# Kernel optimization log

Hardware: AMD Instinct MI355X
Metric: run time of the kernel (lower is better)

Reference implementation:

```python
import jax, jax.numpy as jnp
import numpy as np

L, HS, IN, B, S = 2, 512, 512, 64, 1024

def setup_inputs() -> dict:
    key = jax.random.key(0)
    ks = jax.random.split(key, 11)
    sc = 0.02
    return {
        'x':  jax.random.normal(ks[0], (B, S, IN), jnp.float32),
        'h0': jnp.zeros((L, B, HS), jnp.float32),
        'W1': jax.random.normal(ks[1], (L, 3, 1)) * sc,
        'W2': jax.random.normal(ks[2], (L, HS, IN)) * sc,
        'U1': jax.random.normal(ks[3], (L, 3, 1)) * sc,
        'U2': jax.random.normal(ks[4], (L, HS, HS)) * sc,
        'dW1': jax.random.normal(ks[5], (L, 3, 1)) * sc,
        'dW2': jax.random.normal(ks[6], (L, HS, IN)) * sc,
        'dU1': jax.random.normal(ks[7], (L, 3, 1)) * sc,
        'dU2': jax.random.normal(ks[8], (L, HS, HS)) * sc,
        'b1': jax.random.normal(ks[9], (L, 3 * HS, 1)) * sc,
        'b2': jax.random.normal(ks[10], (L, 3 * HS, 1)) * sc,
    }

def reference(x, h0, W1, W2, U1, U2, dW1, dW2, dU1, dU2, b1, b2):
    # x: (b, s, in); h0: (L, b, HS). All layers read the same x_t (per source).
    b = x.shape[0]
    hs = h0.shape[2]
    bias = b1 + b2                      # (L, 3HS, 1)
    h_init = jnp.transpose(h0, (0, 2, 1))  # (L, HS, b) -- column-major state like gates

    def step(h, x_t):                   # h: (L, HS, b), x_t: (b, in)
        Wx = jnp.einsum('lhi,bi->lhb', W2, x_t)
        dWx = jnp.einsum('lhi,bi->lhb', dW2, x_t)
        Uh = jnp.einsum('lho,lob->lhb', U2, h)
        dUh = jnp.einsum('lho,lob->lhb', dU2, h)
        # kron(A(3,1), M(HS,b)) = stack_g A[g]*M -> (3HS, b)
        gates = (jnp.einsum('lg,lhb->lghb', W1[:, :, 0], Wx)
                 + jnp.einsum('lg,lhb->lghb', U1[:, :, 0], Uh)
                 + jnp.einsum('lg,lhb->lghb', dW1[:, :, 0], dWx)
                 + jnp.einsum('lg,lhb->lghb', dU1[:, :, 0], dUh)
                 ).reshape(h.shape[0], 3 * hs, b) + bias
        r = jax.nn.sigmoid(gates[:, :hs])          # computed but unused, as in source
        z = jax.nn.sigmoid(gates[:, hs:2 * hs])
        n = jnp.tanh(gates[:, 2 * hs:])
        h_new = (1.0 - z) * n + z * h
        return h_new, jnp.transpose(h_new[-1])     # emit last layer, (b, HS)

    h_fin, seq = jax.lax.scan(step, h_init, jnp.transpose(x, (1, 0, 2)))
    hidden_seq = jnp.transpose(seq, (1, 0, 2))     # (b, s, HS)
    state = jnp.transpose(h_fin, (0, 2, 1))        # (L, b, HS)
    return hidden_seq, state
```

## Files before the change

kernel.cpp:

```cpp
#include <hip/hip_runtime.h>


#define HS 512
#define IN_DIM 512
#define BATCH 64
#define SEQ 1024
#define NB 16
#define NDOM 8
#define LDS_ROW 516
#define HROW 520

typedef __attribute__((ext_vector_type(8))) short bf16x8;
typedef __attribute__((ext_vector_type(4))) float f32x4;
typedef unsigned long long u64;
typedef unsigned int u32;
typedef unsigned short ushort_t;

__device__ __forceinline__ ushort_t f2bf(float f) {
  u32 u = __float_as_uint(f);
  u += 0x7FFFu + ((u >> 16) & 1u);
  return (ushort_t)(u >> 16);
}
__device__ __forceinline__ float bf2f(ushort_t s) {
  return __uint_as_float(((u32)s) << 16);
}

__global__ void gru_prep(const float* __restrict__ h0,
                         ushort_t* __restrict__ hbuf,
                         u32* __restrict__ cnt) {
  u32 tid = blockIdx.x * 256u + threadIdx.x;
  if (tid < 2u * BATCH * HS) hbuf[tid] = f2bf(h0[tid]);
  if (tid < NDOM * (SEQ + 1) + 64u) cnt[tid] = 0u;
}

__global__ __launch_bounds__(256, 1) void gru_main(
    const float* __restrict__ x, float* __restrict__ out,
    const float* __restrict__ W1, const float* __restrict__ W2,
    const float* __restrict__ U1, const float* __restrict__ U2,
    const float* __restrict__ dW1, const float* __restrict__ dW2,
    const float* __restrict__ dU1, const float* __restrict__ dU2,
    const float* __restrict__ b1, const float* __restrict__ b2,
    ushort_t* __restrict__ hbuf, u32* __restrict__ cntws) {
  __shared__ __align__(16) float xlds[2][NB * LDS_ROW];
  __shared__ __align__(16) ushort_t hlds[NB * HROW];
  __shared__ u32 mode_sh;

  const int bid    = blockIdx.x;
  const int domain = bid & 7;
  const int slice  = bid >> 3;
  const int layer  = domain & 1;
  const int bg     = domain >> 1;
  const int bo     = bg * NB;
  const int tid    = threadIdx.x;
  const int lane   = tid & 63;
  const int wave   = tid >> 6;
  const int quad   = lane >> 4;
  const int ln     = lane & 15;
  const int hw     = slice * 64 + wave * 16;

  u32* const cnt = cntws + domain * (SEQ + 1);
  u32* const tab = cntws + NDOM * (SEQ + 1);

  if (tid == 0) {
    u32 xcc;
    asm volatile("s_getreg_b32 %0, hwreg(HW_REG_XCC_ID)" : "=s"(xcc));
    __hip_atomic_store(&tab[domain * 8 + slice], 256u + xcc,
                       __ATOMIC_RELAXED, __HIP_MEMORY_SCOPE_AGENT);
    u32 vals[8];
    for (;;) {
      bool ready = true;
#pragma unroll
      for (int i = 0; i < 8; ++i) {
        vals[i] = __hip_atomic_load(&tab[domain * 8 + i],
                                    __ATOMIC_RELAXED, __HIP_MEMORY_SCOPE_AGENT);
        ready = ready && (vals[i] >= 256u);
      }
      if (ready) break;
      __builtin_amdgcn_s_sleep(8);
    }
    u32 m = 1u;
#pragma unroll
    for (int i = 1; i < 8; ++i) m = (vals[i] == vals[0]) ? m : 0u;
    mode_sh = m;
  }
  __syncthreads();
  const bool fast = (mode_sh != 0u);

  const float w1z = W1[layer*3+1], w1n = W1[layer*3+2];
  const float dw1z = dW1[layer*3+1], dw1n = dW1[layer*3+2];
  const float u1z = U1[layer*3+1], u1n = U1[layer*3+2];
  const float du1z = dU1[layer*3+1], du1n = dU1[layer*3+2];
  const int hrow_w = hw + ln;
  const float* W2r  = W2  + ((size_t)layer*HS + hrow_w) * IN_DIM;
  const float* dW2r = dW2 + ((size_t)layer*HS + hrow_w) * IN_DIM;
  const float* U2r  = U2  + ((size_t)layer*HS + hrow_w) * HS;
  const float* dU2r = dU2 + ((size_t)layer*HS + hrow_w) * HS;

  bf16x8 uf[2][16], wf[2][16];
#pragma unroll
  for (int kc = 0; kc < 16; ++kc) {
    const int off = kc*32 + quad*8;
#pragma unroll
    for (int i = 0; i < 8; ++i) {
      float w2 = W2r[off+i], dw2 = dW2r[off+i];
      float u2 = U2r[off+i], du2 = dU2r[off+i];
      wf[0][kc][i] = (short)f2bf(w1z*w2 + dw1z*dw2);
      wf[1][kc][i] = (short)f2bf(w1n*w2 + dw1n*dw2);
      uf[0][kc][i] = (short)f2bf(u1z*u2 + du1z*du2);
      uf[1][kc][i] = (short)f2bf(u1n*u2 + du1n*du2);
    }
  }
  float bz[4], bn[4];
#pragma unroll
  for (int r = 0; r < 4; ++r) {
    const int row = hw + quad*4 + r;
    bz[r] = b1[layer*1536 + 512  + row] + b2[layer*1536 + 512  + row];
    bn[r] = b1[layer*1536 + 1024 + row] + b2[layer*1536 + 1024 + row];
  }

  const int b_lane = bo + ln;
  const size_t slotsz = (size_t)2 * BATCH * HS;
  ushort_t* hl = hbuf + (size_t)layer * BATCH * HS;

#pragma unroll
  for (int i = 0; i < 8; ++i) {
    int bi = wave * 4 + (i >> 1), ch = i & 1;
    const float* g = x + ((size_t)(bo + bi) * SEQ) * IN_DIM + ch * 256 + lane * 4;
    __builtin_amdgcn_global_load_lds(
        (const __attribute__((address_space(1))) void*)g,
        (__attribute__((address_space(3))) void*)&xlds[0][bi * LDS_ROW + ch * 256],
        16, 0, 0);
  }
  asm volatile("s_waitcnt vmcnt(0)" ::: "memory");
  __syncthreads();

  if (fast) {
    for (int t = 0; t < SEQ; ++t) {
      if (t + 1 < SEQ) {
#pragma unroll
        for (int i = 0; i < 8; ++i) {
          int bi = wave * 4 + (i >> 1), ch = i & 1;
          const float* g = x + ((size_t)(bo + bi) * SEQ + (t + 1)) * IN_DIM + ch * 256 + lane * 4;
          __builtin_amdgcn_global_load_lds(
              (const __attribute__((address_space(1))) void*)g,
              (__attribute__((address_space(3))) void*)&xlds[(t + 1) & 1][bi * LDS_ROW + ch * 256],
              16, 0, 0);
        }
      }
      f32x4 accz = {0.f,0.f,0.f,0.f}, accn = {0.f,0.f,0.f,0.f};
      const float* xrow = &xlds[t & 1][ln * LDS_ROW];
#pragma unroll
      for (int kc = 0; kc < 16; ++kc) {
        f32x4 a = *(const f32x4*)(xrow + kc*32 + quad*8);
        f32x4 b = *(const f32x4*)(xrow + kc*32 + quad*8 + 4);
        union { u32 u[4]; bf16x8 v; } xv;
        xv.u[0] = (__float_as_uint(a[1]) & 0xFFFF0000u) | (__float_as_uint(a[0]) >> 16);
        xv.u[1] = (__float_as_uint(a[3]) & 0xFFFF0000u) | (__float_as_uint(a[2]) >> 16);
        xv.u[2] = (__float_as_uint(b[1]) & 0xFFFF0000u) | (__float_as_uint(b[0]) >> 16);
        xv.u[3] = (__float_as_uint(b[3]) & 0xFFFF0000u) | (__float_as_uint(b[2]) >> 16);
        accz = __builtin_amdgcn_mfma_f32_16x16x32_bf16(wf[0][kc], xv.v, accz, 0, 0, 0);
        accn = __builtin_amdgcn_mfma_f32_16x16x32_bf16(wf[1][kc], xv.v, accn, 0, 0, 0);
      }
      if (t > 0) {
        const u32* cp = cnt + t;
        u32 c;
        do {
          asm volatile("global_load_dword %0, %1, off sc0\n\t"
                       "s_waitcnt vmcnt(0)"
                       : "=&v"(c) : "v"(cp) : "memory");
        } while (c != 8u);
      }
      const ushort_t* hsrc = hl + (size_t)(t & 1) * slotsz + (size_t)bo * HS;
#pragma unroll
      for (int r = 0; r < 4; ++r) {
        const int row = wave * 4 + r;
        const ushort_t* g = hsrc + (size_t)row * HS + lane * 8;
        __builtin_amdgcn_global_load_lds(
            (const __attribute__((address_space(1))) void*)g,
            (__attribute__((address_space(3))) void*)&hlds[row * HROW],
            16, 0, 1 );
      }
      asm volatile("s_waitcnt vmcnt(0)" ::: "memory");
      __syncthreads();
      const ushort_t* hr = &hlds[ln * HROW];
#pragma unroll
      for (int kc = 0; kc < 16; ++kc) {
        bf16x8 hv = *(const bf16x8*)(hr + kc*32 + quad*8);
        accz = __builtin_amdgcn_mfma_f32_16x16x32_bf16(uf[0][kc], hv, accz, 0, 0, 0);
        accn = __builtin_amdgcn_mfma_f32_16x16x32_bf16(uf[1][kc], hv, accn, 0, 0, 0);
      }
      u64 hprev = *(const u64*)(hr + hw + quad*4);
      u64 packed = 0;
      f32x4 hnew;
#pragma unroll
      for (int r = 0; r < 4; ++r) {
        float gz = accz[r] + bz[r];
        float gn = accn[r] + bn[r];
        float z  = 1.f / (1.f + __expf(-gz));
        float e2 = __expf(2.f * gn);
        float n  = (e2 - 1.f) / (e2 + 1.f);
        float hp = bf2f((ushort_t)(hprev >> (16 * r)));
        float hn = (1.f - z) * n + z * hp;
        hnew[r] = hn;
        packed |= ((u64)f2bf(hn)) << (16 * r);
      }
      *(u64*)(hl + (size_t)((t + 1) & 1) * slotsz
              + (size_t)b_lane * HS + hw + quad*4) = packed;
      if (layer == 1)
        *(f32x4*)(out + ((size_t)b_lane * SEQ + t) * HS + hw + quad*4) = hnew;
      if (t == SEQ - 1)
        *(f32x4*)(out + (size_t)BATCH * SEQ * HS
                  + ((size_t)layer * BATCH + b_lane) * HS + hw + quad*4) = hnew;
      asm volatile("s_waitcnt vmcnt(0)" ::: "memory");
      __syncthreads();
      if (tid == 0)
        __hip_atomic_fetch_add(cnt + (t + 1), 1u,
                               __ATOMIC_RELAXED, __HIP_MEMORY_SCOPE_WORKGROUP);
    }
  } else {
    for (int t = 0; t < SEQ; ++t) {
      if (t + 1 < SEQ) {
#pragma unroll
        for (int i = 0; i < 8; ++i) {
          int bi = wave * 4 + (i >> 1), ch = i & 1;
          const float* g = x + ((size_t)(bo + bi) * SEQ + (t + 1)) * IN_DIM + ch * 256 + lane * 4;
          __builtin_amdgcn_global_load_lds(
              (const __attribute__((address_space(1))) void*)g,
              (__attribute__((address_space(3))) void*)&xlds[(t + 1) & 1][bi * LDS_ROW + ch * 256],
              16, 0, 0);
        }
      }
      f32x4 accz = {0.f,0.f,0.f,0.f}, accn = {0.f,0.f,0.f,0.f};
      const float* xrow = &xlds[t & 1][ln * LDS_ROW];
#pragma unroll
      for (int kc = 0; kc < 16; ++kc) {
        f32x4 a = *(const f32x4*)(xrow + kc*32 + quad*8);
        f32x4 b = *(const f32x4*)(xrow + kc*32 + quad*8 + 4);
        union { u32 u[4]; bf16x8 v; } xv;
        xv.u[0] = (__float_as_uint(a[1]) & 0xFFFF0000u) | (__float_as_uint(a[0]) >> 16);
        xv.u[1] = (__float_as_uint(a[3]) & 0xFFFF0000u) | (__float_as_uint(a[2]) >> 16);
        xv.u[2] = (__float_as_uint(b[1]) & 0xFFFF0000u) | (__float_as_uint(b[0]) >> 16);
        xv.u[3] = (__float_as_uint(b[3]) & 0xFFFF0000u) | (__float_as_uint(b[2]) >> 16);
        accz = __builtin_amdgcn_mfma_f32_16x16x32_bf16(wf[0][kc], xv.v, accz, 0, 0, 0);
        accn = __builtin_amdgcn_mfma_f32_16x16x32_bf16(wf[1][kc], xv.v, accn, 0, 0, 0);
      }
      if (t > 0) {
        while (__hip_atomic_load(cnt + t, __ATOMIC_RELAXED,
                                 __HIP_MEMORY_SCOPE_AGENT) != 8u)
          __builtin_amdgcn_s_sleep(1);
      }
      const ushort_t* hsrc = hl + (size_t)(t & 1) * slotsz + (size_t)b_lane * HS;
#pragma unroll
      for (int kc = 0; kc < 16; ++kc) {
        const u64* hp = (const u64*)(hsrc + kc*32 + quad*8);
        union { u64 q[2]; bf16x8 v; } hu;
        hu.q[0] = __hip_atomic_load(hp,     __ATOMIC_RELAXED, __HIP_MEMORY_SCOPE_AGENT);
        hu.q[1] = __hip_atomic_load(hp + 1, __ATOMIC_RELAXED, __HIP_MEMORY_SCOPE_AGENT);
        accz = __builtin_amdgcn_mfma_f32_16x16x32_bf16(uf[0][kc], hu.v, accz, 0, 0, 0);
        accn = __builtin_amdgcn_mfma_f32_16x16x32_bf16(uf[1][kc], hu.v, accn, 0, 0, 0);
      }
      u64 hprev = __hip_atomic_load((const u64*)(hsrc + hw + quad*4),
                                    __ATOMIC_RELAXED, __HIP_MEMORY_SCOPE_AGENT);
      u64 packed = 0;
      f32x4 hnew;
#pragma unroll
      for (int r = 0; r < 4; ++r) {
        float gz = accz[r] + bz[r];
        float gn = accn[r] + bn[r];
        float z  = 1.f / (1.f + __expf(-gz));
        float e2 = __expf(2.f * gn);
        float n  = (e2 - 1.f) / (e2 + 1.f);
        float hp = bf2f((ushort_t)(hprev >> (16 * r)));
        float hn = (1.f - z) * n + z * hp;
        hnew[r] = hn;
        packed |= ((u64)f2bf(hn)) << (16 * r);
      }
      __hip_atomic_store((u64*)(hl + (size_t)((t + 1) & 1) * slotsz
                                + (size_t)b_lane * HS + hw + quad*4),
                         packed, __ATOMIC_RELAXED, __HIP_MEMORY_SCOPE_AGENT);
      if (layer == 1)
        *(f32x4*)(out + ((size_t)b_lane * SEQ + t) * HS + hw + quad*4) = hnew;
      if (t == SEQ - 1)
        *(f32x4*)(out + (size_t)BATCH * SEQ * HS
                  + ((size_t)layer * BATCH + b_lane) * HS + hw + quad*4) = hnew;
      asm volatile("s_waitcnt vmcnt(0)" ::: "memory");
      __syncthreads();
      if (tid == 0)
        __hip_atomic_fetch_add(cnt + (t + 1), 1u,
                               __ATOMIC_RELAXED, __HIP_MEMORY_SCOPE_AGENT);
    }
  }
}

extern "C" void kernel_launch(void* const* d_in, const int* in_sizes, int n_in,
                              void* d_out, int out_size, void* d_ws, size_t ws_size,
                              hipStream_t stream) {
  const float* x   = (const float*)d_in[0];
  const float* h0  = (const float*)d_in[1];
  const float* W1  = (const float*)d_in[2];
  const float* W2  = (const float*)d_in[3];
  const float* U1  = (const float*)d_in[4];
  const float* U2  = (const float*)d_in[5];
  const float* dW1 = (const float*)d_in[6];
  const float* dW2 = (const float*)d_in[7];
  const float* dU1 = (const float*)d_in[8];
  const float* dU2 = (const float*)d_in[9];
  const float* b1  = (const float*)d_in[10];
  const float* b2  = (const float*)d_in[11];

  char* ws = (char*)d_ws;
  ushort_t* hbuf = (ushort_t*)ws;
  u32*      cnt  = (u32*)(ws + 262144);

  gru_prep<<<257, 256, 0, stream>>>(h0, hbuf, cnt);
  gru_main<<<64, 256, 0, stream>>>(x, (float*)d_out,
                                   W1, W2, U1, U2, dW1, dW2, dU1, dU2, b1, b2,
                                   hbuf, cnt);
}
```

Baseline: 3.760 ms.

## Load recurrent state directly into registers and split MFMA accumulators

Replaces the per-step global-to-LDS staging of the hidden state, and the barrier that followed it, with direct per-lane dwordx4 global loads into registers. The loads are issued in two halves so the first half's MFMAs overlap the second half's loads. Each accumulator is split into two independent chains to shorten MFMA dependency latency. The previous hidden value is also kept in a register instead of being re-read. The cost is more VGPRs and redundant global reads, since each lane now fetches its own copy of the h rows.

```diff
diff --git a/kernel.cpp b/kernel.cpp
--- a/kernel.cpp
+++ b/kernel.cpp
@@ -8,7 +8,6 @@
 #define NB 16
 #define NDOM 8
 #define LDS_ROW 516
-#define HROW 520
 
 typedef __attribute__((ext_vector_type(8))) short bf16x8;
 typedef __attribute__((ext_vector_type(4))) float f32x4;
@@ -42,7 +41,6 @@
     const float* __restrict__ b1, const float* __restrict__ b2,
     ushort_t* __restrict__ hbuf, u32* __restrict__ cntws) {
   __shared__ __align__(16) float xlds[2][NB * LDS_ROW];
-  __shared__ __align__(16) ushort_t hlds[NB * HROW];
   __shared__ u32 mode_sh;
 
   const int bid    = blockIdx.x;
@@ -135,6 +133,8 @@
   __syncthreads();
 
   if (fast) {
+    u64 hprev_reg = *(const u64*)(hl + (size_t)b_lane * HS + hw + quad*4);
+
     for (int t = 0; t < SEQ; ++t) {
       if (t + 1 < SEQ) {
 #pragma unroll
@@ -147,19 +147,28 @@
               16, 0, 0);
         }
       }
-      f32x4 accz = {0.f,0.f,0.f,0.f}, accn = {0.f,0.f,0.f,0.f};
+      f32x4 az0 = {0.f,0.f,0.f,0.f}, az1 = {0.f,0.f,0.f,0.f};
+      f32x4 an0 = {0.f,0.f,0.f,0.f}, an1 = {0.f,0.f,0.f,0.f};
       const float* xrow = &xlds[t & 1][ln * LDS_ROW];
 #pragma unroll
-      for (int kc = 0; kc < 16; ++kc) {
-        f32x4 a = *(const f32x4*)(xrow + kc*32 + quad*8);
-        f32x4 b = *(const f32x4*)(xrow + kc*32 + quad*8 + 4);
-        union { u32 u[4]; bf16x8 v; } xv;
-        xv.u[0] = (__float_as_uint(a[1]) & 0xFFFF0000u) | (__float_as_uint(a[0]) >> 16);
-        xv.u[1] = (__float_as_uint(a[3]) & 0xFFFF0000u) | (__float_as_uint(a[2]) >> 16);
-        xv.u[2] = (__float_as_uint(b[1]) & 0xFFFF0000u) | (__float_as_uint(b[0]) >> 16);
-        xv.u[3] = (__float_as_uint(b[3]) & 0xFFFF0000u) | (__float_as_uint(b[2]) >> 16);
-        accz = __builtin_amdgcn_mfma_f32_16x16x32_bf16(wf[0][kc], xv.v, accz, 0, 0, 0);
-        accn = __builtin_amdgcn_mfma_f32_16x16x32_bf16(wf[1][kc], xv.v, accn, 0, 0, 0);
+      for (int kc = 0; kc < 16; kc += 2) {
+        f32x4 a0 = *(const f32x4*)(xrow + kc*32 + quad*8);
+        f32x4 b0 = *(const f32x4*)(xrow + kc*32 + quad*8 + 4);
+        f32x4 a1 = *(const f32x4*)(xrow + (kc+1)*32 + quad*8);
+        f32x4 b1v = *(const f32x4*)(xrow + (kc+1)*32 + quad*8 + 4);
+        union { u32 u[4]; bf16x8 v; } x0, x1;
+        x0.u[0] = (__float_as_uint(a0[1]) & 0xFFFF0000u) | (__float_as_uint(a0[0]) >> 16);
+        x0.u[1] = (__float_as_uint(a0[3]) & 0xFFFF0000u) | (__float_as_uint(a0[2]) >> 16);
+        x0.u[2] = (__float_as_uint(b0[1]) & 0xFFFF0000u) | (__float_as_uint(b0[0]) >> 16);
+        x0.u[3] = (__float_as_uint(b0[3]) & 0xFFFF0000u) | (__float_as_uint(b0[2]) >> 16);
+        x1.u[0] = (__float_as_uint(a1[1]) & 0xFFFF0000u) | (__float_as_uint(a1[0]) >> 16);
+        x1.u[1] = (__float_as_uint(a1[3]) & 0xFFFF0000u) | (__float_as_uint(a1[2]) >> 16);
+        x1.u[2] = (__float_as_uint(b1v[1]) & 0xFFFF0000u) | (__float_as_uint(b1v[0]) >> 16);
+        x1.u[3] = (__float_as_uint(b1v[3]) & 0xFFFF0000u) | (__float_as_uint(b1v[2]) >> 16);
+        az0 = __builtin_amdgcn_mfma_f32_16x16x32_bf16(wf[0][kc],   x0.v, az0, 0, 0, 0);
+        an0 = __builtin_amdgcn_mfma_f32_16x16x32_bf16(wf[1][kc],   x0.v, an0, 0, 0, 0);
+        az1 = __builtin_amdgcn_mfma_f32_16x16x32_bf16(wf[0][kc+1], x1.v, az1, 0, 0, 0);
+        an1 = __builtin_amdgcn_mfma_f32_16x16x32_bf16(wf[1][kc+1], x1.v, an1, 0, 0, 0);
       }
       if (t > 0) {
         const u32* cp = cnt + t;
@@ -170,40 +179,50 @@
                        : "=&v"(c) : "v"(cp) : "memory");
         } while (c != 8u);
       }
-      const ushort_t* hsrc = hl + (size_t)(t & 1) * slotsz + (size_t)bo * HS;
-#pragma unroll
-      for (int r = 0; r < 4; ++r) {
-        const int row = wave * 4 + r;
-        const ushort_t* g = hsrc + (size_t)row * HS + lane * 8;
-        __builtin_amdgcn_global_load_lds(
-            (const __attribute__((address_space(1))) void*)g,
-            (__attribute__((address_space(3))) void*)&hlds[row * HROW],
-            16, 0, 1 );
-      }
+      const ushort_t* hp = hl + (size_t)(t & 1) * slotsz
+                           + (size_t)b_lane * HS + quad * 8;
+      bf16x8 hva[8], hvb[8];
+#define HLD(D, OFF) asm volatile("global_load_dwordx4 %0, %1, off offset:" OFF " sc0" \
+                                 : "=v"(D) : "v"(hp) : "memory");
+      HLD(hva[0],"0")    HLD(hva[1],"64")   HLD(hva[2],"128")  HLD(hva[3],"192")
+      HLD(hva[4],"256")  HLD(hva[5],"320")  HLD(hva[6],"384")  HLD(hva[7],"448")
       asm volatile("s_waitcnt vmcnt(0)" ::: "memory");
-      __syncthreads();
-      const ushort_t* hr = &hlds[ln * HROW];
-#pragma unroll
-      for (int kc = 0; kc < 16; ++kc) {
-        bf16x8 hv = *(const bf16x8*)(hr + kc*32 + quad*8);
-        accz = __builtin_amdgcn_mfma_f32_16x16x32_bf16(uf[0][kc], hv, accz, 0, 0, 0);
-        accn = __builtin_amdgcn_mfma_f32_16x16x32_bf16(uf[1][kc], hv, accn, 0, 0, 0);
-      }
-      u64 hprev = *(const u64*)(hr + hw + quad*4);
+      __builtin_amdgcn_sched_barrier(0);
+      HLD(hvb[0],"512")  HLD(hvb[1],"576")  HLD(hvb[2],"640")  HLD(hvb[3],"704")
+      HLD(hvb[4],"768")  HLD(hvb[5],"832")  HLD(hvb[6],"896")  HLD(hvb[7],"960")
+#undef HLD
+      __builtin_amdgcn_sched_barrier(0);
+#pragma unroll
+      for (int kc = 0; kc < 8; kc += 2) {
+        az0 = __builtin_amdgcn_mfma_f32_16x16x32_bf16(uf[0][kc],   hva[kc],   az0, 0, 0, 0);
+        an0 = __builtin_amdgcn_mfma_f32_16x16x32_bf16(uf[1][kc],   hva[kc],   an0, 0, 0, 0);
+        az1 = __builtin_amdgcn_mfma_f32_16x16x32_bf16(uf[0][kc+1], hva[kc+1], az1, 0, 0, 0);
+        an1 = __builtin_amdgcn_mfma_f32_16x16x32_bf16(uf[1][kc+1], hva[kc+1], an1, 0, 0, 0);
+      }
+      asm volatile("s_waitcnt vmcnt(0)" ::: "memory");
+      __builtin_amdgcn_sched_barrier(0);
+#pragma unroll
+      for (int kc = 8; kc < 16; kc += 2) {
+        az0 = __builtin_amdgcn_mfma_f32_16x16x32_bf16(uf[0][kc],   hvb[kc-8], az0, 0, 0, 0);
+        an0 = __builtin_amdgcn_mfma_f32_16x16x32_bf16(uf[1][kc],   hvb[kc-8], an0, 0, 0, 0);
+        az1 = __builtin_amdgcn_mfma_f32_16x16x32_bf16(uf[0][kc+1], hvb[kc-7], az1, 0, 0, 0);
+        an1 = __builtin_amdgcn_mfma_f32_16x16x32_bf16(uf[1][kc+1], hvb[kc-7], an1, 0, 0, 0);
+      }
       u64 packed = 0;
       f32x4 hnew;
 #pragma unroll
       for (int r = 0; r < 4; ++r) {
-        float gz = accz[r] + bz[r];
-        float gn = accn[r] + bn[r];
+        float gz = az0[r] + az1[r] + bz[r];
+        float gn = an0[r] + an1[r] + bn[r];
         float z  = 1.f / (1.f + __expf(-gz));
         float e2 = __expf(2.f * gn);
         float n  = (e2 - 1.f) / (e2 + 1.f);
-        float hp = bf2f((ushort_t)(hprev >> (16 * r)));
-        float hn = (1.f - z) * n + z * hp;
+        float hp2 = bf2f((ushort_t)(hprev_reg >> (16 * r)));
+        float hn = (1.f - z) * n + z * hp2;
         hnew[r] = hn;
         packed |= ((u64)f2bf(hn)) << (16 * r);
       }
+      hprev_reg = packed;
       *(u64*)(hl + (size_t)((t + 1) & 1) * slotsz
               + (size_t)b_lane * HS + hw + quad*4) = packed;
       if (layer == 1)
```

After: 4.990 ms. 32.7% more time.
